# Performance work log

Hardware: AMD Instinct MI355X
Metric: run time of the kernel (lower is better)

## Reference

```python
import jax, jax.numpy as jnp
import numpy as np
import math

HEAD_DEPTH = 16
CLIP = 10.0
NEG_INF = 1.0e10
# combined scale: (1/sqrt(head_depth)) * log_50(400)
SCALE = (math.log(400.0) / math.log(50.0)) / math.sqrt(HEAD_DEPTH)


def setup_inputs() -> dict:
    key = jax.random.key(0)
    kq, kk, kv, km = jax.random.split(key, 4)
    B, H, S, D = 4, 8, 2048, HEAD_DEPTH
    Q = jax.random.normal(kq, (B, H, S, D), dtype=jnp.float32)
    K = jax.random.normal(kk, (B, H, S, D), dtype=jnp.float32)
    V = jax.random.normal(kv, (B, H, S, D), dtype=jnp.float32)
    # mask: (B, n_nodes, 1) bool; True -> masked (logit set to -inf)
    mask = jax.random.randint(km, (B, S, 1), 0, 2) == 1
    return {"Q": Q, "K": K, "V": V, "mask": mask}


def reference(Q, K, V, mask):
    # logits: (B, H, q_seq, k_seq)
    logits = jnp.einsum("bhqd,bhkd->bhqk", Q, K) * SCALE
    logits = CLIP * jnp.tanh(logits)  # tanh clip
    # mask[:, None, None, :, 0] -> (B, 1, 1, k_seq), True gets -inf
    m = mask[:, None, None, :, 0]
    logits = jnp.where(m, -NEG_INF, logits)
    probs = jax.nn.softmax(logits, axis=-1)
    return jnp.einsum("bhqk,bhkd->bhqd", probs, V)
```

## Files before the change

kernel.cpp:

```cpp
#include <hip/hip_runtime.h>


typedef __fp16 h2 __attribute__((ext_vector_type(2)));
typedef __fp16 h4 __attribute__((ext_vector_type(4)));
typedef float  f4 __attribute__((ext_vector_type(4)));

#define SEQ 2048
#define NBH 32
#define TPB 128
#define KWS_BYTES ((size_t)NBH * TPB * 64 * 8)
#define VWS_BYTES KWS_BYTES
#define BIAS_BYTES ((size_t)4 * SEQ * 4)
#define WS_NEEDED (KWS_BYTES + VWS_BYTES + BIAS_BYTES)

__device__ __forceinline__ float fast_exp2(float x) {
#if __has_builtin(__builtin_amdgcn_exp2f)
    return __builtin_amdgcn_exp2f(x);
#else
    return exp2f(x);
#endif
}

__device__ __forceinline__ float dot2acc(h2 a, float accv) {
#if __has_builtin(__builtin_amdgcn_fdot2)
    const h2 one = {(__fp16)1.0f, (__fp16)1.0f};
    return __builtin_amdgcn_fdot2(a, one, accv, false);
#else
    return accv + (float)a[0] + (float)a[1];
#endif
}

__global__ __launch_bounds__(256) void attn_prep(
    const float* __restrict__ Kp, const float* __restrict__ Vp,
    const int* __restrict__ maskp,
    __fp16* __restrict__ Kws, __fp16* __restrict__ Vws, float* __restrict__ biasws)
{
    const int tid = threadIdx.x;
    const int T   = blockIdx.x * 4 + (tid >> 6);
    const int l   = tid & 63;
    const int bh  = T >> 7;
    const int t   = T & (TPB - 1);
    const int c   = l & 15;
    const int g   = l >> 4;
    const size_t base = (size_t)bh * (SEQ * 16);

    {
        f4 kv = *(const f4*)(Kp + base + (size_t)(t * 16 + c) * 16 + 4 * g);
        h2 k0 = __builtin_amdgcn_cvt_pkrtz(kv[0], kv[1]);
        h2 k1 = __builtin_amdgcn_cvt_pkrtz(kv[2], kv[3]);
        h4 kh; kh[0] = k0[0]; kh[1] = k0[1]; kh[2] = k1[0]; kh[3] = k1[1];
        *(h4*)(Kws + ((size_t)T * 64 + l) * 4) = kh;
    }
    {
        const float* vrow = Vp + base + (size_t)(t * 16 + 4 * g) * 16 + c;
        h2 p0 = __builtin_amdgcn_cvt_pkrtz(vrow[0],  vrow[16]);
        h2 p1 = __builtin_amdgcn_cvt_pkrtz(vrow[32], vrow[48]);
        h4 vh; vh[0] = p0[0]; vh[1] = p0[1]; vh[2] = p1[0]; vh[3] = p1[1];
        *(h4*)(Vws + ((size_t)T * 64 + l) * 4) = vh;
    }
    if (blockIdx.x < 32) {
        const int idx = blockIdx.x * 256 + tid;
        biasws[idx] = maskp[idx] ? -60.0f : 0.0f;
    }
}

__global__ __launch_bounds__(512, 8) void attn_v4(
    const float* __restrict__ Qp, const __fp16* __restrict__ Kws,
    const __fp16* __restrict__ Vws, const float* __restrict__ biasws,
    float* __restrict__ out)
{
    __shared__ __align__(16) _Float16 Kbuf[2][4096];
    __shared__ __align__(16) _Float16 Vbuf[2][4096];
    __shared__ __align__(16) float    Bbuf[2][256];

    const int bid  = blockIdx.x;
    const int bh   = bid >> 5;
    const int qblk = bid & 31;
    const int b    = bh >> 3;
    const int tid  = threadIdx.x;
    const int wave = tid >> 6;
    const int lane = tid & 63;
    const int qt   = wave & 3;
    const int kg   = wave >> 2;
    const int c    = lane & 15;
    const int g    = lane >> 4;

    const size_t base  = (size_t)bh * (SEQ * 16);
    const int    qbase = qblk * 64 + qt * 16;
    const float  c1 = 1.1047809f;
    const float  c2 = -28.8539008f;

    h4 qfrag;
    {
        f4 qv = *(const f4*)(Qp + base + (size_t)(qbase + c) * 16 + 4 * g);
        h2 lo = __builtin_amdgcn_cvt_pkrtz(c1 * qv[0], c1 * qv[1]);
        h2 hi = __builtin_amdgcn_cvt_pkrtz(c1 * qv[2], c1 * qv[3]);
        qfrag[0] = lo[0]; qfrag[1] = lo[1]; qfrag[2] = hi[0]; qfrag[3] = hi[1];
    }

    const f4* ksrc = (const f4*)(Kws + (size_t)bh * TPB * 256);
    const f4* vsrc = (const f4*)(Vws + (size_t)bh * TPB * 256);
    const float* bsrc = biasws + (size_t)b * SEQ;

    f4 kpre = ksrc[tid];
    f4 vpre = vsrc[tid];
    float bpre = (tid < 256) ? bsrc[tid] : 0.0f;
    *(f4*)&Kbuf[0][tid * 8] = kpre;
    *(f4*)&Vbuf[0][tid * 8] = vpre;
    if (tid < 256) Bbuf[0][tid] = bpre;
    kpre = ksrc[512 + tid];
    vpre = vsrc[512 + tid];
    if (tid < 256) bpre = bsrc[256 + tid];
    __syncthreads();

    f4 acc = {0.f, 0.f, 0.f, 0.f};
    float dsum = 0.f;

    for (int r = 0; r < 8; ++r) {
        const int cb = r & 1, nb = (r + 1) & 1;
        if (r < 7) {
            *(f4*)&Kbuf[nb][tid * 8] = kpre;
            *(f4*)&Vbuf[nb][tid * 8] = vpre;
            if (tid < 256) Bbuf[nb][tid] = bpre;
        }
        if (r < 6) {
            kpre = ksrc[(r + 2) * 512 + tid];
            vpre = vsrc[(r + 2) * 512 + tid];
            if (tid < 256) bpre = bsrc[(r + 2) * 256 + tid];
        }

        const _Float16* Kc = &Kbuf[cb][kg * 2048];
        const _Float16* Vc = &Vbuf[cb][kg * 2048];
        const float*    Bc = &Bbuf[cb][kg * 128];

        #pragma unroll
        for (int t = 0; t < 8; ++t) {
            h4 afrag = *(const h4*)(Kc + t * 256 + lane * 4);
            f4 s = __builtin_amdgcn_mfma_f32_16x16x16f16(
                afrag, qfrag, (f4){0.f, 0.f, 0.f, 0.f}, 0, 0, 0);

            f4 b4 = *(const f4*)(Bc + t * 16 + 4 * g);
            float p[4];
            #pragma unroll
            for (int i = 0; i < 4; ++i) {
                float tt = fast_exp2(s[i]);
                float w  = __builtin_amdgcn_rcpf(1.0f + tt);
                p[i] = fast_exp2(__builtin_fmaf(c2, w, b4[i]));
            }
            h2 plo = __builtin_amdgcn_cvt_pkrtz(p[0], p[1]);
            h2 phi = __builtin_amdgcn_cvt_pkrtz(p[2], p[3]);
            dsum = dot2acc(plo, dsum);
            dsum = dot2acc(phi, dsum);
            h4 pf; pf[0] = plo[0]; pf[1] = plo[1]; pf[2] = phi[0]; pf[3] = phi[1];

            h4 vfrag = *(const h4*)(Vc + t * 256 + lane * 4);
            acc = __builtin_amdgcn_mfma_f32_16x16x16f16(pf, vfrag, acc, 0, 0, 0);
        }
        __syncthreads();
    }

    dsum += __shfl_xor(dsum, 16);
    dsum += __shfl_xor(dsum, 32);

    float* ex = (float*)&Kbuf[0][0];
    const int slot = (qt * 64 + lane) * 5;
    if (kg == 1) {
        ex[slot + 0] = acc[0]; ex[slot + 1] = acc[1];
        ex[slot + 2] = acc[2]; ex[slot + 3] = acc[3];
        ex[slot + 4] = dsum;
    }
    __syncthreads();
    if (kg == 0) {
        const float dT = dsum + ex[slot + 4];
        #pragma unroll
        for (int i = 0; i < 4; ++i) {
            const float denom = __shfl(dT, 4 * g + i);
            out[base + (size_t)(qbase + 4 * g + i) * 16 + c] =
                (acc[i] + ex[slot + i]) / denom;
        }
    }
}

#define KROW 20
#define VROW 520

__global__ __launch_bounds__(512, 8) void attn_fwd_v3(
    const float* __restrict__ Qp, const float* __restrict__ Kp,
    const float* __restrict__ Vp, const int* __restrict__ maskp,
    float* __restrict__ out)
{
    __shared__ __align__(16) _Float16 Klds[512 * KROW];
    __shared__ __align__(16) _Float16 Vt[16 * VROW];
    __shared__ __align__(16) float biasf[512];

    const int bid  = blockIdx.x;
    const int bh   = bid >> 5;
    const int qblk = bid & 31;
    const int b    = bh >> 3;
    const int tid  = threadIdx.x;
    const int wave = tid >> 6;
    const int lane = tid & 63;
    const int qt   = wave & 3;
    const int kg   = wave >> 2;
    const int c    = lane & 15;
    const int g    = lane >> 4;

    const size_t base = (size_t)bh * (SEQ * 16);
    const int qbase = qblk * 64 + qt * 16;
    const float c1 = 1.1047809f;
    const float c2 = -28.8539008f;

    h4 qfrag;
    {
        f4 qv = *(const f4*)(Qp + base + (size_t)(qbase + c) * 16 + 4 * g);
        h2 lo = __builtin_amdgcn_cvt_pkrtz(c1 * qv[0], c1 * qv[1]);
        h2 hi = __builtin_amdgcn_cvt_pkrtz(c1 * qv[2], c1 * qv[3]);
        qfrag[0] = lo[0]; qfrag[1] = lo[1]; qfrag[2] = hi[0]; qfrag[3] = hi[1];
    }

    f4 acc = {0.f, 0.f, 0.f, 0.f};
    float dsum = 0.f;
    const int kgb = kg * 256;

    for (int round = 0; round < 4; ++round) {
        {
            const float* Kc = Kp + base + (size_t)round * (512 * 16);
            const float* Vc = Vp + base + (size_t)round * (512 * 16);
            #pragma unroll
            for (int j = 0; j < 4; ++j) {
                const int i = j * 512 + tid;
                f4 kv = *(const f4*)(Kc + (size_t)i * 4);
                f4 vv = *(const f4*)(Vc + (size_t)i * 4);
                const int key = i >> 2;
                const int dq  = (i & 3) * 4;
                h2 k0 = __builtin_amdgcn_cvt_pkrtz(kv[0], kv[1]);
                h2 k1 = __builtin_amdgcn_cvt_pkrtz(kv[2], kv[3]);
                h4 kh; kh[0] = k0[0]; kh[1] = k0[1]; kh[2] = k1[0]; kh[3] = k1[1];
                *(h4*)&Klds[key * KROW + dq] = kh;
                #pragma unroll
                for (int e = 0; e < 4; ++e)
                    Vt[(dq + e) * VROW + key] = (_Float16)vv[e];
            }
            biasf[tid] = maskp[(size_t)b * SEQ + round * 512 + tid] ? -60.0f : 0.0f;
        }
        __syncthreads();

        #pragma unroll
        for (int t = 0; t < 16; ++t) {
            const int kb = kgb + t * 16;
            h4 afrag = *(const h4*)&Klds[(kb + c) * KROW + 4 * g];
            f4 s = __builtin_amdgcn_mfma_f32_16x16x16f16(
                afrag, qfrag, (f4){0.f, 0.f, 0.f, 0.f}, 0, 0, 0);
            f4 b4 = *(const f4*)&biasf[kb + 4 * g];
            float p[4];
            #pragma unroll
            for (int i = 0; i < 4; ++i) {
                float tt = fast_exp2(s[i]);
                float w  = __builtin_amdgcn_rcpf(1.0f + tt);
                p[i] = fast_exp2(__builtin_fmaf(c2, w, b4[i]));
            }
            h2 plo = __builtin_amdgcn_cvt_pkrtz(p[0], p[1]);
            h2 phi = __builtin_amdgcn_cvt_pkrtz(p[2], p[3]);
            dsum = dot2acc(plo, dsum);
            dsum = dot2acc(phi, dsum);
            h4 pf; pf[0] = plo[0]; pf[1] = plo[1]; pf[2] = phi[0]; pf[3] = phi[1];
            h4 vfrag = *(const h4*)&Vt[c * VROW + kb + 4 * g];
            acc = __builtin_amdgcn_mfma_f32_16x16x16f16(pf, vfrag, acc, 0, 0, 0);
        }
        __syncthreads();
    }

    dsum += __shfl_xor(dsum, 16);
    dsum += __shfl_xor(dsum, 32);

    float* ex = (float*)Klds;
    const int slot = (qt * 64 + lane) * 5;
    if (kg == 1) {
        ex[slot + 0] = acc[0]; ex[slot + 1] = acc[1];
        ex[slot + 2] = acc[2]; ex[slot + 3] = acc[3];
        ex[slot + 4] = dsum;
    }
    __syncthreads();
    if (kg == 0) {
        const float dT = dsum + ex[slot + 4];
        #pragma unroll
        for (int i = 0; i < 4; ++i) {
            const float denom = __shfl(dT, 4 * g + i);
            out[base + (size_t)(qbase + 4 * g + i) * 16 + c] =
                (acc[i] + ex[slot + i]) / denom;
        }
    }
}

extern "C" void kernel_launch(void* const* d_in, const int* in_sizes, int n_in,
                              void* d_out, int out_size, void* d_ws, size_t ws_size,
                              hipStream_t stream) {
    const float* Q    = (const float*)d_in[0];
    const float* K    = (const float*)d_in[1];
    const float* V    = (const float*)d_in[2];
    const int*   mask = (const int*)d_in[3];
    float* out = (float*)d_out;

    if (ws_size >= WS_NEEDED) {
        __fp16* Kws = (__fp16*)d_ws;
        __fp16* Vws = (__fp16*)((char*)d_ws + KWS_BYTES);
        float*  Bws = (float*)((char*)d_ws + KWS_BYTES + VWS_BYTES);
        attn_prep<<<dim3(1024), dim3(256), 0, stream>>>(K, V, mask, Kws, Vws, Bws);
        attn_v4<<<dim3(1024), dim3(512), 0, stream>>>(Q, Kws, Vws, Bws, out);
    } else {
        attn_fwd_v3<<<dim3(1024), dim3(512), 0, stream>>>(Q, K, V, mask, out);
    }
}
```

Measured before the change: 106.6 us.

## Compact unmasked keys via prefix scan and skip masked key blocks

Adds a per-batch scan kernel that compacts the indices of unmasked keys and builds a bias marking the padded tail. The prep kernel now gathers K and V rows through these indices, and the attention kernel loops only over the number of 256-key blocks holding unmasked keys. With about half the keys masked, this roughly halves the attention work. The cost is an extra small launch, gathered (less coalesced) loads in prep, and a data-dependent loop count.

```diff
diff --git a/kernel.cpp b/kernel.cpp
--- a/kernel.cpp
+++ b/kernel.cpp
@@ -11,7 +11,9 @@
 #define KWS_BYTES ((size_t)NBH * TPB * 64 * 8)
 #define VWS_BYTES KWS_BYTES
 #define BIAS_BYTES ((size_t)4 * SEQ * 4)
-#define WS_NEEDED (KWS_BYTES + VWS_BYTES + BIAS_BYTES)
+#define IDX_BYTES  ((size_t)4 * SEQ * 4)
+#define META_BYTES 64
+#define WS_NEEDED (KWS_BYTES + VWS_BYTES + BIAS_BYTES + IDX_BYTES + META_BYTES)
 
 __device__ __forceinline__ float fast_exp2(float x) {
 #if __has_builtin(__builtin_amdgcn_exp2f)
@@ -30,44 +32,86 @@
 #endif
 }
 
+__global__ __launch_bounds__(256) void attn_scan(
+    const int* __restrict__ maskp, int* __restrict__ idxws,
+    float* __restrict__ biasws, int* __restrict__ meta)
+{
+    __shared__ int partial[256];
+    const int b   = blockIdx.x;
+    const int tid = threadIdx.x;
+
+    int keep[8], cnt = 0;
+    #pragma unroll
+    for (int j = 0; j < 8; ++j) {
+        keep[j] = (maskp[b * SEQ + tid * 8 + j] == 0);
+        cnt += keep[j];
+    }
+    partial[tid] = cnt;
+    __syncthreads();
+    for (int off = 1; off < 256; off <<= 1) {
+        int add = (tid >= off) ? partial[tid - off] : 0;
+        __syncthreads();
+        partial[tid] += add;
+        __syncthreads();
+    }
+    const int total = partial[255];
+    int pos = partial[tid] - cnt;
+    #pragma unroll
+    for (int j = 0; j < 8; ++j) {
+        if (keep[j]) idxws[b * SEQ + pos++] = tid * 8 + j;
+    }
+    for (int i = tid; i < SEQ; i += 256) {
+        biasws[b * SEQ + i] = (i < total) ? 0.0f : -1.0e30f;
+        if (i >= total) idxws[b * SEQ + i] = 0;
+    }
+    if (tid == 0) {
+        int nr = (total + 255) >> 8;
+        meta[b] = nr < 1 ? 1 : nr;
+    }
+}
+
 __global__ __launch_bounds__(256) void attn_prep(
     const float* __restrict__ Kp, const float* __restrict__ Vp,
-    const int* __restrict__ maskp,
-    __fp16* __restrict__ Kws, __fp16* __restrict__ Vws, float* __restrict__ biasws)
+    const int* __restrict__ idxws,
+    __fp16* __restrict__ Kws, __fp16* __restrict__ Vws)
 {
     const int tid = threadIdx.x;
     const int T   = blockIdx.x * 4 + (tid >> 6);
     const int l   = tid & 63;
     const int bh  = T >> 7;
     const int t   = T & (TPB - 1);
+    const int b   = bh >> 3;
     const int c   = l & 15;
     const int g   = l >> 4;
     const size_t base = (size_t)bh * (SEQ * 16);
-
-    {
-        f4 kv = *(const f4*)(Kp + base + (size_t)(t * 16 + c) * 16 + 4 * g);
+    const int*   idx  = idxws + (size_t)b * SEQ;
+
+    {
+        const int krow = idx[t * 16 + c];
+        f4 kv = *(const f4*)(Kp + base + (size_t)krow * 16 + 4 * g);
         h2 k0 = __builtin_amdgcn_cvt_pkrtz(kv[0], kv[1]);
         h2 k1 = __builtin_amdgcn_cvt_pkrtz(kv[2], kv[3]);
         h4 kh; kh[0] = k0[0]; kh[1] = k0[1]; kh[2] = k1[0]; kh[3] = k1[1];
         *(h4*)(Kws + ((size_t)T * 64 + l) * 4) = kh;
     }
     {
-        const float* vrow = Vp + base + (size_t)(t * 16 + 4 * g) * 16 + c;
-        h2 p0 = __builtin_amdgcn_cvt_pkrtz(vrow[0],  vrow[16]);
-        h2 p1 = __builtin_amdgcn_cvt_pkrtz(vrow[32], vrow[48]);
+        const int v0 = idx[t * 16 + 4 * g + 0];
+        const int v1 = idx[t * 16 + 4 * g + 1];
+        const int v2 = idx[t * 16 + 4 * g + 2];
+        const int v3 = idx[t * 16 + 4 * g + 3];
+        h2 p0 = __builtin_amdgcn_cvt_pkrtz(Vp[base + (size_t)v0 * 16 + c],
+                                           Vp[base + (size_t)v1 * 16 + c]);
+        h2 p1 = __builtin_amdgcn_cvt_pkrtz(Vp[base + (size_t)v2 * 16 + c],
+                                           Vp[base + (size_t)v3 * 16 + c]);
         h4 vh; vh[0] = p0[0]; vh[1] = p0[1]; vh[2] = p1[0]; vh[3] = p1[1];
         *(h4*)(Vws + ((size_t)T * 64 + l) * 4) = vh;
     }
-    if (blockIdx.x < 32) {
-        const int idx = blockIdx.x * 256 + tid;
-        biasws[idx] = maskp[idx] ? -60.0f : 0.0f;
-    }
-}
-
-__global__ __launch_bounds__(512, 8) void attn_v4(
+}
+
+__global__ __launch_bounds__(512, 8) void attn_v5(
     const float* __restrict__ Qp, const __fp16* __restrict__ Kws,
     const __fp16* __restrict__ Vws, const float* __restrict__ biasws,
-    float* __restrict__ out)
+    const int* __restrict__ meta, float* __restrict__ out)
 {
     __shared__ __align__(16) _Float16 Kbuf[2][4096];
     __shared__ __align__(16) _Float16 Vbuf[2][4096];
@@ -90,6 +134,8 @@
     const float  c1 = 1.1047809f;
     const float  c2 = -28.8539008f;
 
+    const int nr = meta[b];
+
     h4 qfrag;
     {
         f4 qv = *(const f4*)(Qp + base + (size_t)(qbase + c) * 16 + 4 * g);
@@ -108,22 +154,25 @@
     *(f4*)&Kbuf[0][tid * 8] = kpre;
     *(f4*)&Vbuf[0][tid * 8] = vpre;
     if (tid < 256) Bbuf[0][tid] = bpre;
-    kpre = ksrc[512 + tid];
-    vpre = vsrc[512 + tid];
-    if (tid < 256) bpre = bsrc[256 + tid];
+    {
+        const int r1 = (1 < nr) ? 1 : (nr - 1);
+        kpre = ksrc[r1 * 512 + tid];
+        vpre = vsrc[r1 * 512 + tid];
+        if (tid < 256) bpre = bsrc[r1 * 256 + tid];
+    }
     __syncthreads();
 
     f4 acc = {0.f, 0.f, 0.f, 0.f};
     float dsum = 0.f;
 
-    for (int r = 0; r < 8; ++r) {
-        const int cb = r & 1, nb = (r + 1) & 1;
-        if (r < 7) {
+    for (int r = 0; r < nr; ++r) {
+        const int cb = r & 1, nb = cb ^ 1;
+        if (r + 1 < nr) {
             *(f4*)&Kbuf[nb][tid * 8] = kpre;
             *(f4*)&Vbuf[nb][tid * 8] = vpre;
             if (tid < 256) Bbuf[nb][tid] = bpre;
         }
-        if (r < 6) {
+        if (r + 2 < nr) {
             kpre = ksrc[(r + 2) * 512 + tid];
             vpre = vsrc[(r + 2) * 512 + tid];
             if (tid < 256) bpre = bsrc[(r + 2) * 256 + tid];
@@ -302,11 +351,15 @@
     float* out = (float*)d_out;
 
     if (ws_size >= WS_NEEDED) {
-        __fp16* Kws = (__fp16*)d_ws;
-        __fp16* Vws = (__fp16*)((char*)d_ws + KWS_BYTES);
-        float*  Bws = (float*)((char*)d_ws + KWS_BYTES + VWS_BYTES);
-        attn_prep<<<dim3(1024), dim3(256), 0, stream>>>(K, V, mask, Kws, Vws, Bws);
-        attn_v4<<<dim3(1024), dim3(512), 0, stream>>>(Q, Kws, Vws, Bws, out);
+        char* p = (char*)d_ws;
+        __fp16* Kws = (__fp16*)p;                       p += KWS_BYTES;
+        __fp16* Vws = (__fp16*)p;                       p += VWS_BYTES;
+        float*  Bws = (float*)p;                        p += BIAS_BYTES;
+        int*    Iws = (int*)p;                          p += IDX_BYTES;
+        int*    Mws = (int*)p;
+        attn_scan<<<dim3(4), dim3(256), 0, stream>>>(mask, Iws, Bws, Mws);
+        attn_prep<<<dim3(1024), dim3(256), 0, stream>>>(K, V, Iws, Kws, Vws);
+        attn_v5<<<dim3(1024), dim3(512), 0, stream>>>(Q, Kws, Vws, Bws, Mws, out);
     } else {
         attn_fwd_v3<<<dim3(1024), dim3(512), 0, stream>>>(Q, K, V, mask, out);
     }
```

New measurement: 93.38 us. 12.4% less time.
